# Performance work log

Measured on AMD Instinct MI355X. Metric: run time of the kernel, lower is better.

## Reference

```python
import jax, jax.numpy as jnp
import numpy as np

B, T, V = 4, 2048, 2048
D, H, L = 512, 8, 4
HD = D // H


def setup_inputs() -> dict:
    key = jax.random.key(0)
    ks = jax.random.split(key, 8)
    inp = {
        "x": jax.random.normal(ks[0], (B, T, V), dtype=jnp.float32),
        "token_embedding": jax.random.normal(ks[1], (D, V), dtype=jnp.float32),
        "position_embedding": jax.random.normal(ks[2], (T, D), dtype=jnp.float32),
        "Wk": jax.random.normal(ks[3], (L, D, D), dtype=jnp.float32),
        "Wq": jax.random.normal(ks[4], (L, D, D), dtype=jnp.float32),
        "Wv": jax.random.normal(ks[5], (L, D, D), dtype=jnp.float32),
        "Wp": jax.random.normal(ks[6], (L, D, D), dtype=jnp.float32),
        "readout": jax.random.normal(ks[7], (V, D), dtype=jnp.float32),
    }
    return inp


def _attention_block(h, wk, wq, wv, wp):
    # h: [B, T, D]; weights [D, D] (inner_dim == D since head_dim*num_heads == D)
    b, t, c = h.shape
    s = c ** (-0.5)

    def proj(w):
        # F.linear(h, w) = h @ w.T -> [B,T,D] -> [B,H,T,HD], scaled by C^{-1/2}
        return (jnp.einsum('btc,dc->btd', h, w) * s).reshape(b, t, H, HD).transpose(0, 2, 1, 3)

    q, k, v = proj(wq), proj(wk), proj(wv)
    scores = jnp.einsum('bhqd,bhkd->bhqk', q, k) * (HD ** (-0.5))  # [B,H,T,T]
    attn = jax.nn.softmax(scores, axis=-1)
    out = jnp.einsum('bhqk,bhkd->bhqd', attn, v)  # [B,H,T,HD]
    out = out.transpose(0, 2, 1, 3).reshape(b, t, c)
    # projection.size(-1) == inner_dim == D
    return jnp.einsum('btc,oc->bto', out, wp) * (c ** (-0.5))


def reference(x, token_embedding, position_embedding, Wk, Wq, Wv, Wp, readout):
    b, t, c = x.shape  # c == vocab_size
    tok = jnp.einsum('btv,dv->btd', x, token_embedding) * (c ** (-0.5))
    h = tok + position_embedding[:t]
    for l in range(L):
        h = _attention_block(h, Wk[l], Wq[l], Wv[l], Wp[l])
    # logits on last token; readout.size(-1) == D
    logits = jnp.einsum('bd,vd->bv', h[:, -1, :], readout) * (D ** (-0.5))
    return logits
```

## Files before the change

### kernel.cpp

```cpp
#include <hip/hip_runtime.h>
#include <math.h>

typedef __attribute__((ext_vector_type(4)))  float    f32x4;
typedef __attribute__((ext_vector_type(16))) float    f32x16;
typedef __attribute__((ext_vector_type(2)))  _Float16 f16x2;
typedef __attribute__((ext_vector_type(4)))  _Float16 f16x4;
typedef __attribute__((ext_vector_type(8)))  _Float16 f16x8;
typedef __attribute__((ext_vector_type(4)))  unsigned u32x4;

constexpr int Bc  = 4;
constexpr int Tc  = 2048;
constexpr int Vc  = 2048;
constexpr int Dc  = 512;
constexpr int Hc  = 8;
constexpr int HDc = 64;
constexpr int Lc  = 4;
constexpr size_t SZe = (size_t)Bc * Tc * Dc;

constexpr float SM_C = 12.0f;

__device__ __forceinline__ void gload_lds16(const _Float16* g, _Float16* s) {
    __builtin_amdgcn_global_load_lds(
        (const __attribute__((address_space(1))) void*)g,
        (__attribute__((address_space(3))) void*)s,
        16, 0, 0);
}

__device__ __forceinline__ unsigned cvt_pk_u(float a, float b) {
    return __builtin_bit_cast(unsigned, __builtin_amdgcn_cvt_pkrtz(a, b));
}

__global__ __launch_bounds__(256) void cvt_k(
    const float* __restrict__ in, _Float16* __restrict__ out, int n4)
{
    for (int i = blockIdx.x * 256 + threadIdx.x; i < n4; i += gridDim.x * 256) {
        float4 v = ((const float4*)in)[i];
        f16x4 h = {(_Float16)v.x, (_Float16)v.y, (_Float16)v.z, (_Float16)v.w};
        *(f16x4*)&out[(size_t)i * 4] = h;
    }
}

__global__ __launch_bounds__(256) void cvtW_k(
    const float* __restrict__ a, const float* __restrict__ b,
    const float* __restrict__ c, const float* __restrict__ d,
    _Float16* __restrict__ oa, _Float16* __restrict__ ob,
    _Float16* __restrict__ oc, _Float16* __restrict__ od, int n4)
{
    const float* in; _Float16* out;
    switch (blockIdx.y) {
        case 0:  in = a; out = oa; break;
        case 1:  in = b; out = ob; break;
        case 2:  in = c; out = oc; break;
        default: in = d; out = od; break;
    }
    for (int i = blockIdx.x * 256 + threadIdx.x; i < n4; i += gridDim.x * 256) {
        float4 v = ((const float4*)in)[i];
        f16x4 h = {(_Float16)v.x, (_Float16)v.y, (_Float16)v.z, (_Float16)v.w};
        *(f16x4*)&out[(size_t)i * 4] = h;
    }
}


template<bool QKV>
__global__ __launch_bounds__(256) void gemm_f16(
    const _Float16* __restrict__ A,
    const _Float16* __restrict__ W0, const _Float16* __restrict__ W1,
    const _Float16* __restrict__ W2,
    void* __restrict__ C0, const float* __restrict__ pos,
    int K, float scA, float scB, int mstep, int moff, int ybase)
{
    __shared__ __align__(16) _Float16 LA[2][128 * 64];
    __shared__ __align__(16) _Float16 LB[2][64 * 64];

    const int tid = threadIdx.x;
    const int w  = tid >> 6, l = tid & 63;
    const int li = l & 15,  lg = l >> 4;
    const int wm = w >> 1,  wn = w & 1;
    const int m0 = (blockIdx.x * mstep + moff) * 128;
    const int y  = blockIdx.y + ybase;

    int sec = 0, n0;
    const _Float16* Wb;
    if (QKV) {
        sec = y >> 3; n0 = (y & 7) * 64;
        Wb = (sec == 0) ? W0 : ((sec == 1) ? W1 : W2);
    } else {
        n0 = y * 64; Wb = W0;
    }
    const float scale = (sec == 0) ? scA : scB;

    const _Float16* srcA[4];
    const _Float16* srcB[2];
#pragma unroll
    for (int i = 0; i < 4; ++i) {
        const int d = i * 4096 + tid * 16;
        const int r = d >> 7, cb = (d & 127) ^ ((r & 7) << 4);
        srcA[i] = A + (size_t)(m0 + r) * K + (cb >> 1);
    }
#pragma unroll
    for (int i = 0; i < 2; ++i) {
        const int d = i * 4096 + tid * 16;
        const int r = d >> 7, cb = (d & 127) ^ ((r & 7) << 4);
        srcB[i] = Wb + (size_t)(n0 + r) * K + (cb >> 1);
    }

    auto stage = [&](int b) {
#pragma unroll
        for (int i = 0; i < 4; ++i) { gload_lds16(srcA[i], &LA[b][i * 2048 + tid * 8]); srcA[i] += 64; }
#pragma unroll
        for (int i = 0; i < 2; ++i) { gload_lds16(srcB[i], &LB[b][i * 2048 + tid * 8]); srcB[i] += 64; }
    };

    f32x4 acc[4][2];
#pragma unroll
    for (int i = 0; i < 4; ++i)
#pragma unroll
        for (int j = 0; j < 2; ++j) acc[i][j] = (f32x4){0.f, 0.f, 0.f, 0.f};

    auto compute = [&](int b) {
        const char* Ab = (const char*)&LA[b][0];
        const char* Bb = (const char*)&LB[b][0];
        f16x8 af[4][2], bf[2][2];
#pragma unroll
        for (int mb = 0; mb < 4; ++mb) {
            const int row = wm * 64 + mb * 16 + li, sz = (row & 7) << 4;
#pragma unroll
            for (int fi = 0; fi < 2; ++fi)
                af[mb][fi] = *(const f16x8*)(Ab + row * 128 + ((fi * 64 + lg * 16) ^ sz));
        }
#pragma unroll
        for (int nb = 0; nb < 2; ++nb) {
            const int row = wn * 32 + nb * 16 + li, sz = (row & 7) << 4;
#pragma unroll
            for (int fi = 0; fi < 2; ++fi)
                bf[nb][fi] = *(const f16x8*)(Bb + row * 128 + ((fi * 64 + lg * 16) ^ sz));
        }
#pragma unroll
        for (int mb = 0; mb < 4; ++mb)
#pragma unroll
            for (int nb = 0; nb < 2; ++nb)
#pragma unroll
                for (int fi = 0; fi < 2; ++fi)
                    acc[mb][nb] = __builtin_amdgcn_mfma_f32_16x16x32_f16(
                        af[mb][fi], bf[nb][fi], acc[mb][nb], 0, 0, 0);
    };

    const int NTk = K >> 6;
    stage(0);
    for (int kt = 0; kt < NTk; ++kt) {
        const int cur = kt & 1;
        if (kt + 1 < NTk) {
            stage(cur ^ 1);
            asm volatile("s_waitcnt vmcnt(6)" ::: "memory");
        } else {
            asm volatile("s_waitcnt vmcnt(0)" ::: "memory");
        }
        __builtin_amdgcn_s_barrier();
        __builtin_amdgcn_sched_barrier(0);
        compute(cur);
        __builtin_amdgcn_s_barrier();
        __builtin_amdgcn_sched_barrier(0);
    }

#pragma unroll
    for (int mb = 0; mb < 4; ++mb) {
#pragma unroll
        for (int nb = 0; nb < 2; ++nb) {
            const int mbase = m0 + wm * 64 + mb * 16 + lg * 4;
            const int nc    = n0 + wn * 32 + nb * 16 + li;
            if (QKV && sec == 2) {
                const int t0 = mbase & (Tc - 1);
                const int bh2 = (mbase >> 11) * Hc + (nc >> 6), d = nc & 63;
                f16x4 vv;
#pragma unroll
                for (int r = 0; r < 4; ++r) vv[r] = (_Float16)(acc[mb][nb][r] * scale);
                _Float16* vf = (_Float16*)C0 + 2 * SZe;
                const size_t adr =
                    (((size_t)bh2 * 32 + (t0 >> 6)) * 8 + (d >> 5) * 4 + ((t0 >> 4) & 3)) * 512
                    + ((d & 31) + 32 * ((t0 >> 3) & 1)) * 8 + (t0 & 7);
                *(f16x4*)&vf[adr] = vv;
            } else if (QKV && sec == 1) {
                _Float16* kf = (_Float16*)C0 + SZe;
                const int t0 = mbase & (Tc - 1);
                const int bh2 = (mbase >> 11) * Hc + (nc >> 6), d = nc & 63;
                const size_t adr0 =
                    (((size_t)bh2 * 32 + (t0 >> 6)) * 8 + ((t0 >> 5) & 1) * 4 + (d >> 4)) * 512
                    + ((t0 & 31) + 32 * ((d >> 3) & 1)) * 8 + (d & 7);
#pragma unroll
                for (int r = 0; r < 4; ++r)
                    kf[adr0 + (size_t)r * 8] = (_Float16)(acc[mb][nb][r] * scale);
            } else if (QKV) {
                _Float16* outp = (_Float16*)C0;
#pragma unroll
                for (int r = 0; r < 4; ++r) {
                    const int m = mbase + r, bb2 = m >> 11, t = m & (Tc - 1);
                    outp[(((size_t)bb2 * Hc + (nc >> 6)) * Tc + t) * HDc + (nc & 63)] =
                        (_Float16)(acc[mb][nb][r] * scale);
                }
            } else {
                _Float16* outp = (_Float16*)C0;
#pragma unroll
                for (int r = 0; r < 4; ++r) {
                    const int m = mbase + r;
                    float val = acc[mb][nb][r] * scale;
                    if (pos) val += pos[(size_t)(m & (Tc - 1)) * Dc + nc];
                    outp[(size_t)m * Dc + nc] = (_Float16)val;
                }
            }
        }
    }
}

__global__ __launch_bounds__(256) void attn_mfma(
    const _Float16* __restrict__ Qh, const _Float16* __restrict__ Kf,
    const _Float16* __restrict__ Vf, _Float16* __restrict__ o, int qtoff)
{
    __shared__ float cm[4224];

    const int bid = blockIdx.x;
    const int bh  = bid & 31;
    const int qt  = (bid >> 5) + qtoff;
    const int hh  = bh & (Hc - 1);
    const int bb  = bh >> 3;
    const int tid = threadIdx.x;
    const int w   = tid >> 6;
    const int l   = tid & 63;
    const int li  = l & 31, lg2 = l >> 5;
    const int qhalf = w & 1, khalf = w >> 1;
    const int q0  = qt * 64 + qhalf * 32;

    const _Float16* Qb = Qh + (size_t)bh * Tc * HDc;
    f16x8 qf[4];
#pragma unroll
    for (int fi = 0; fi < 4; ++fi)
        qf[fi] = *(const f16x8*)&Qb[(size_t)(q0 + li) * HDc + fi * 16 + lg2 * 8];

    const _Float16* Kb  = Kf + (size_t)bh * Tc * HDc + (khalf * 4) * 512 + l * 8;
    const _Float16* Vb0 = Vf + (size_t)bh * Tc * HDc + (khalf * 2) * 512 + l * 8;
    const _Float16* Vb1 = Vb0 + 4 * 512;

    f32x16 oacc0, oacc1, lacc, sinit;
#pragma unroll
    for (int i = 0; i < 16; ++i) { oacc0[i] = 0.f; oacc1[i] = 0.f; lacc[i] = 0.f; sinit[i] = -SM_C; }
    f16x8 ones;
#pragma unroll
    for (int i = 0; i < 8; ++i) ones[i] = (_Float16)1.f;

    f16x8 kfr[4], vfr[4];
#pragma unroll
    for (int fi = 0; fi < 4; ++fi) kfr[fi] = *(const f16x8*)(Kb + fi * 512);
#pragma unroll
    for (int m = 0; m < 2; ++m) {
        vfr[m]     = *(const f16x8*)(Vb0 + m * 512);
        vfr[2 + m] = *(const f16x8*)(Vb1 + m * 512);
    }
    Kb += 4096; Vb0 += 4096; Vb1 += 4096;

    constexpr int NT = Tc / 64;
    for (int kt = 0; kt < NT; ++kt) {
        __builtin_amdgcn_s_setprio(1);
        f32x16 s = __builtin_amdgcn_mfma_f32_32x32x16_f16(kfr[0], qf[0], sinit, 0, 0, 0);
        s = __builtin_amdgcn_mfma_f32_32x32x16_f16(kfr[1], qf[1], s, 0, 0, 0);
        s = __builtin_amdgcn_mfma_f32_32x32x16_f16(kfr[2], qf[2], s, 0, 0, 0);
        s = __builtin_amdgcn_mfma_f32_32x32x16_f16(kfr[3], qf[3], s, 0, 0, 0);
        __builtin_amdgcn_s_setprio(0);

        if (kt + 1 < NT) {
#pragma unroll
            for (int fi = 0; fi < 4; ++fi) kfr[fi] = *(const f16x8*)(Kb + fi * 512);
            Kb += 4096;
        }

        unsigned cc[8];
#pragma unroll
        for (int g = 0; g < 4; ++g) {
            float p0 = __builtin_amdgcn_exp2f(s[4 * g + 0]);
            float p1 = __builtin_amdgcn_exp2f(s[4 * g + 1]);
            float p2 = __builtin_amdgcn_exp2f(s[4 * g + 2]);
            float p3 = __builtin_amdgcn_exp2f(s[4 * g + 3]);
            cc[2 * g]     = cvt_pk_u(p0, p1);
            cc[2 * g + 1] = cvt_pk_u(p2, p3);
        }

        f16x8 Bf[2];
#pragma unroll
        for (int m = 0; m < 2; ++m) {
            auto u = __builtin_amdgcn_permlane32_swap(cc[m * 4 + 0], cc[m * 4 + 2], false, false);
            auto v = __builtin_amdgcn_permlane32_swap(cc[m * 4 + 1], cc[m * 4 + 3], false, false);
            u32x4 b4 = (u32x4){u[0], v[0], u[1], v[1]};
            Bf[m] = __builtin_bit_cast(f16x8, b4);
        }

        __builtin_amdgcn_s_setprio(1);
        lacc  = __builtin_amdgcn_mfma_f32_32x32x16_f16(ones,   Bf[0], lacc,  0, 0, 0);
        oacc0 = __builtin_amdgcn_mfma_f32_32x32x16_f16(vfr[0], Bf[0], oacc0, 0, 0, 0);
        oacc0 = __builtin_amdgcn_mfma_f32_32x32x16_f16(vfr[1], Bf[1], oacc0, 0, 0, 0);
        lacc  = __builtin_amdgcn_mfma_f32_32x32x16_f16(ones,   Bf[1], lacc,  0, 0, 0);
        oacc1 = __builtin_amdgcn_mfma_f32_32x32x16_f16(vfr[2], Bf[0], oacc1, 0, 0, 0);
        oacc1 = __builtin_amdgcn_mfma_f32_32x32x16_f16(vfr[3], Bf[1], oacc1, 0, 0, 0);
        __builtin_amdgcn_s_setprio(0);

        if (kt + 1 < NT) {
#pragma unroll
            for (int m = 0; m < 2; ++m) {
                vfr[m]     = *(const f16x8*)(Vb0 + m * 512);
                vfr[2 + m] = *(const f16x8*)(Vb1 + m * 512);
            }
            Vb0 += 4096; Vb1 += 4096;
        }
    }

    const float lrun_w = lacc[0];
    const int cbase = qhalf * (64 * 33) + l * 33;
    if (khalf == 1) {
#pragma unroll
        for (int i = 0; i < 16; ++i) cm[cbase + i]      = oacc0[i];
#pragma unroll
        for (int i = 0; i < 16; ++i) cm[cbase + 16 + i] = oacc1[i];
        cm[cbase + 32] = lrun_w;
    }
    __syncthreads();
    if (khalf == 0) {
#pragma unroll
        for (int i = 0; i < 16; ++i) oacc0[i] += cm[cbase + i];
#pragma unroll
        for (int i = 0; i < 16; ++i) oacc1[i] += cm[cbase + 16 + i];
        const float inv = 1.f / (lrun_w + cm[cbase + 32]);

        _Float16* op = o + ((size_t)(bb * Tc + q0 + li) * Dc + hh * HDc);
#pragma unroll
        for (int g = 0; g < 4; ++g) {
            const int d0 = 8 * g + 4 * lg2;
            f16x4 r0 = {(_Float16)(oacc0[4 * g + 0] * inv), (_Float16)(oacc0[4 * g + 1] * inv),
                        (_Float16)(oacc0[4 * g + 2] * inv), (_Float16)(oacc0[4 * g + 3] * inv)};
            f16x4 r1 = {(_Float16)(oacc1[4 * g + 0] * inv), (_Float16)(oacc1[4 * g + 1] * inv),
                        (_Float16)(oacc1[4 * g + 2] * inv), (_Float16)(oacc1[4 * g + 3] * inv)};
            *(f16x4*)(op + d0)      = r0;
            *(f16x4*)(op + 32 + d0) = r1;
        }
    }
}

__global__ __launch_bounds__(256) void readout_k(
    const _Float16* __restrict__ h, const float* __restrict__ ro,
    float* __restrict__ out, float scale)
{
    const int idx = blockIdx.x * 256 + threadIdx.x;
    const int vv  = idx & (Vc - 1);
    const int bb  = idx >> 11;
    const _Float16* hp = h + (size_t)(bb * Tc + (Tc - 1)) * Dc;
    const float* rp = ro + (size_t)vv * Dc;
    float ax = 0.f, ay = 0.f, az = 0.f, aw = 0.f;
#pragma unroll 8
    for (int i = 0; i < Dc / 4; ++i) {
        f16x4  hv = *(const f16x4*)(hp + i * 4);
        float4 rv = *(const float4*)(rp + i * 4);
        ax = fmaf((float)hv[0], rv.x, ax);
        ay = fmaf((float)hv[1], rv.y, ay);
        az = fmaf((float)hv[2], rv.z, az);
        aw = fmaf((float)hv[3], rv.w, aw);
    }
    out[idx] = ((ax + ay) + (az + aw)) * scale;
}

extern "C" void kernel_launch(void* const* d_in, const int* in_sizes, int n_in,
                              void* d_out, int out_size, void* d_ws, size_t ws_size,
                              hipStream_t stream)
{
    const float* x    = (const float*)d_in[0];
    const float* temb = (const float*)d_in[1];
    const float* pemb = (const float*)d_in[2];
    const float* Wk   = (const float*)d_in[3];
    const float* Wq   = (const float*)d_in[4];
    const float* Wv   = (const float*)d_in[5];
    const float* Wp   = (const float*)d_in[6];
    const float* ro   = (const float*)d_in[7];
    float* out = (float*)d_out;

    _Float16* h16    = (_Float16*)d_ws;
    _Float16* temb16 = h16 + SZe;
    _Float16* wq16   = temb16 + (size_t)Dc * Vc;
    _Float16* wk16   = wq16 + (size_t)Lc * Dc * Dc;
    _Float16* wv16   = wk16 + (size_t)Lc * Dc * Dc;
    _Float16* wp16   = wv16 + (size_t)Lc * Dc * Dc;
    _Float16* o16    = wp16 + (size_t)Lc * Dc * Dc;
    _Float16* qh     = o16 + SZe;
    _Float16* khF    = qh + SZe;
    _Float16* vhF    = khF + SZe;
    _Float16* x16    = o16;

    const float s_emb  = 1.0f / sqrtf((float)Vc);
    const float s_proj = 1.0f / sqrtf((float)Dc);
    const float s_q    = s_proj * 0.125f * 1.44269504f;

    const int W4 = Lc * Dc * Dc / 4;
    cvt_k<<<2048, 256, 0, stream>>>(x, x16, (int)SZe);
    cvt_k<<<512, 256, 0, stream>>>(temb, temb16, Dc * Vc / 4);
    cvtW_k<<<dim3(512, 4), 256, 0, stream>>>(Wq, Wk, Wv, Wp,
                                             wq16, wk16, wv16, wp16, W4);

    gemm_f16<false><<<dim3(64, 8), 256, 0, stream>>>(
        x16, temb16, nullptr, nullptr, h16, pemb, Vc, s_emb, s_emb, 1, 0, 0);

    const size_t WOFF = (size_t)Dc * Dc;
    for (int lyr = 0; lyr < Lc; ++lyr) {
        const bool last = (lyr == Lc - 1);
        if (!last) {
            gemm_f16<true><<<dim3(64, 24), 256, 0, stream>>>(
                h16, wq16 + lyr * WOFF, wk16 + lyr * WOFF, wv16 + lyr * WOFF,
                qh, nullptr, Dc, s_q, s_proj, 1, 0, 0);

            attn_mfma<<<Bc * Hc * (Tc / 64), 256, 0, stream>>>(qh, khF, vhF, o16, 0);

            gemm_f16<false><<<dim3(64, 8), 256, 0, stream>>>(
                o16, wp16 + lyr * WOFF, nullptr, nullptr, h16, nullptr,
                Dc, s_proj, s_proj, 1, 0, 0);
        } else {
            gemm_f16<true><<<dim3(64, 16), 256, 0, stream>>>(
                h16, wq16 + lyr * WOFF, wk16 + lyr * WOFF, wv16 + lyr * WOFF,
                qh, nullptr, Dc, s_q, s_proj, 1, 0, 8);
            gemm_f16<true><<<dim3(4, 8), 256, 0, stream>>>(
                h16, wq16 + lyr * WOFF, wk16 + lyr * WOFF, wv16 + lyr * WOFF,
                qh, nullptr, Dc, s_q, s_proj, 16, 15, 0);

            attn_mfma<<<Bc * Hc, 256, 0, stream>>>(qh, khF, vhF, o16, 31);

            gemm_f16<false><<<dim3(4, 8), 256, 0, stream>>>(
                o16, wp16 + lyr * WOFF, nullptr, nullptr, h16, nullptr,
                Dc, s_proj, s_proj, 16, 15, 0);
        }
    }

    readout_k<<<(Bc * Vc) / 256, 256, 0, stream>>>(h16, ro, out, s_proj);
}
```

Baseline: 383.0 us.

## Split attention key tiles across eight waves with two-stage LDS reduction

The attention kernel now runs 512 threads per block. The new set of four waves processes alternating 64-key tiles, so each wave walks half as many K/V tiles. Partial outputs and row sums are combined through two LDS reduction rounds before normalization and the store. This is meant to shorten the per-block serial loop and raise wave count for latency hiding. The cost is more register and LDS pressure per block, extra barriers, and possibly fewer resident blocks per CU.

```diff
diff --git a/kernel.cpp b/kernel.cpp
--- a/kernel.cpp
+++ b/kernel.cpp
@@ -211,11 +211,11 @@
     }
 }
 
-__global__ __launch_bounds__(256) void attn_mfma(
+__global__ __launch_bounds__(512) void attn_mfma(
     const _Float16* __restrict__ Qh, const _Float16* __restrict__ Kf,
     const _Float16* __restrict__ Vf, _Float16* __restrict__ o, int qtoff)
 {
-    __shared__ float cm[4224];
+    __shared__ float cm[4 * 64 * 33];
 
     const int bid = blockIdx.x;
     const int bh  = bid & 31;
@@ -226,7 +226,7 @@
     const int w   = tid >> 6;
     const int l   = tid & 63;
     const int li  = l & 31, lg2 = l >> 5;
-    const int qhalf = w & 1, khalf = w >> 1;
+    const int qhalf = w & 1, khalf = (w >> 1) & 1, ktp = w >> 2;
     const int q0  = qt * 64 + qhalf * 32;
 
     const _Float16* Qb = Qh + (size_t)bh * Tc * HDc;
@@ -235,8 +235,10 @@
     for (int fi = 0; fi < 4; ++fi)
         qf[fi] = *(const f16x8*)&Qb[(size_t)(q0 + li) * HDc + fi * 16 + lg2 * 8];
 
-    const _Float16* Kb  = Kf + (size_t)bh * Tc * HDc + (khalf * 4) * 512 + l * 8;
-    const _Float16* Vb0 = Vf + (size_t)bh * Tc * HDc + (khalf * 2) * 512 + l * 8;
+    const _Float16* Kb  = Kf + (size_t)bh * Tc * HDc + (size_t)ktp * 4096
+                          + (khalf * 4) * 512 + l * 8;
+    const _Float16* Vb0 = Vf + (size_t)bh * Tc * HDc + (size_t)ktp * 4096
+                          + (khalf * 2) * 512 + l * 8;
     const _Float16* Vb1 = Vb0 + 4 * 512;
 
     f32x16 oacc0, oacc1, lacc, sinit;
@@ -254,10 +256,10 @@
         vfr[m]     = *(const f16x8*)(Vb0 + m * 512);
         vfr[2 + m] = *(const f16x8*)(Vb1 + m * 512);
     }
-    Kb += 4096; Vb0 += 4096; Vb1 += 4096;
+    Kb += 8192; Vb0 += 8192; Vb1 += 8192;
 
     constexpr int NT = Tc / 64;
-    for (int kt = 0; kt < NT; ++kt) {
+    for (int kt = ktp; kt < NT; kt += 2) {
         __builtin_amdgcn_s_setprio(1);
         f32x16 s = __builtin_amdgcn_mfma_f32_32x32x16_f16(kfr[0], qf[0], sinit, 0, 0, 0);
         s = __builtin_amdgcn_mfma_f32_32x32x16_f16(kfr[1], qf[1], s, 0, 0, 0);
@@ -265,10 +267,10 @@
         s = __builtin_amdgcn_mfma_f32_32x32x16_f16(kfr[3], qf[3], s, 0, 0, 0);
         __builtin_amdgcn_s_setprio(0);
 
-        if (kt + 1 < NT) {
+        if (kt + 2 < NT) {
 #pragma unroll
             for (int fi = 0; fi < 4; ++fi) kfr[fi] = *(const f16x8*)(Kb + fi * 512);
-            Kb += 4096;
+            Kb += 8192;
         }
 
         unsigned cc[8];
@@ -300,32 +302,52 @@
         oacc1 = __builtin_amdgcn_mfma_f32_32x32x16_f16(vfr[3], Bf[1], oacc1, 0, 0, 0);
         __builtin_amdgcn_s_setprio(0);
 
-        if (kt + 1 < NT) {
+        if (kt + 2 < NT) {
 #pragma unroll
             for (int m = 0; m < 2; ++m) {
                 vfr[m]     = *(const f16x8*)(Vb0 + m * 512);
                 vfr[2 + m] = *(const f16x8*)(Vb1 + m * 512);
             }
-            Vb0 += 4096; Vb1 += 4096;
-        }
-    }
-
-    const float lrun_w = lacc[0];
-    const int cbase = qhalf * (64 * 33) + l * 33;
-    if (khalf == 1) {
-#pragma unroll
-        for (int i = 0; i < 16; ++i) cm[cbase + i]      = oacc0[i];
-#pragma unroll
-        for (int i = 0; i < 16; ++i) cm[cbase + 16 + i] = oacc1[i];
-        cm[cbase + 32] = lrun_w;
+            Vb0 += 8192; Vb1 += 8192;
+        }
+    }
+
+    float lrun = lacc[0];
+    const int slot = qhalf * 2 + khalf;
+    float* cs = cm + slot * (64 * 33) + l * 33;
+
+    if (ktp == 1) {
+#pragma unroll
+        for (int i = 0; i < 16; ++i) cs[i]      = oacc0[i];
+#pragma unroll
+        for (int i = 0; i < 16; ++i) cs[16 + i] = oacc1[i];
+        cs[32] = lrun;
     }
     __syncthreads();
-    if (khalf == 0) {
-#pragma unroll
-        for (int i = 0; i < 16; ++i) oacc0[i] += cm[cbase + i];
-#pragma unroll
-        for (int i = 0; i < 16; ++i) oacc1[i] += cm[cbase + 16 + i];
-        const float inv = 1.f / (lrun_w + cm[cbase + 32]);
+    if (ktp == 0) {
+#pragma unroll
+        for (int i = 0; i < 16; ++i) oacc0[i] += cs[i];
+#pragma unroll
+        for (int i = 0; i < 16; ++i) oacc1[i] += cs[16 + i];
+        lrun += cs[32];
+    }
+    __syncthreads();
+
+    float* cs2 = cm + (qhalf * 2 + 1) * (64 * 33) + l * 33;
+    if (ktp == 0 && khalf == 1) {
+#pragma unroll
+        for (int i = 0; i < 16; ++i) cs2[i]      = oacc0[i];
+#pragma unroll
+        for (int i = 0; i < 16; ++i) cs2[16 + i] = oacc1[i];
+        cs2[32] = lrun;
+    }
+    __syncthreads();
+    if (ktp == 0 && khalf == 0) {
+#pragma unroll
+        for (int i = 0; i < 16; ++i) oacc0[i] += cs2[i];
+#pragma unroll
+        for (int i = 0; i < 16; ++i) oacc1[i] += cs2[16 + i];
+        const float inv = 1.f / (lrun + cs2[32]);
 
         _Float16* op = o + ((size_t)(bb * Tc + q0 + li) * Dc + hh * HDc);
 #pragma unroll
@@ -410,7 +432,7 @@
                 h16, wq16 + lyr * WOFF, wk16 + lyr * WOFF, wv16 + lyr * WOFF,
                 qh, nullptr, Dc, s_q, s_proj, 1, 0, 0);
 
-            attn_mfma<<<Bc * Hc * (Tc / 64), 256, 0, stream>>>(qh, khF, vhF, o16, 0);
+            attn_mfma<<<Bc * Hc * (Tc / 64), 512, 0, stream>>>(qh, khF, vhF, o16, 0);
 
             gemm_f16<false><<<dim3(64, 8), 256, 0, stream>>>(
                 o16, wp16 + lyr * WOFF, nullptr, nullptr, h16, nullptr,
@@ -423,7 +445,7 @@
                 h16, wq16 + lyr * WOFF, wk16 + lyr * WOFF, wv16 + lyr * WOFF,
                 qh, nullptr, Dc, s_q, s_proj, 16, 15, 0);
 
-            attn_mfma<<<Bc * Hc, 256, 0, stream>>>(qh, khF, vhF, o16, 31);
+            attn_mfma<<<Bc * Hc, 512, 0, stream>>>(qh, khF, vhF, o16, 31);
 
             gemm_f16<false><<<dim3(4, 8), 256, 0, stream>>>(
                 o16, wp16 + lyr * WOFF, nullptr, nullptr, h16, nullptr,
```

Measured after the change: 381.0 us. No clear change (-0.5%).

## Halve GEMM M-tile to 64 rows and merge conversion kernels into one launch

Applied to the files above, without the earlier changes.

Shrinks the GEMM block tile from 128x64 to 64x64, so per-wave accumulators, LDS staging and the vmcnt wait count drop and the grid doubles. This gives more blocks to spread across the many CUs for these fairly small GEMMs (M=8192, N=512). The last-layer launches that compute only the final token's 64-row tile get updated mstep/moff values. The three fp32-to-fp16 conversion launches become a single 6-way kernel to cut launch overhead. The cost is lower per-block operand reuse and more global/L2 traffic for the weight tiles.

```diff
diff --git a/kernel.cpp b/kernel.cpp
--- a/kernel.cpp
+++ b/kernel.cpp
@@ -30,9 +30,23 @@
     return __builtin_bit_cast(unsigned, __builtin_amdgcn_cvt_pkrtz(a, b));
 }
 
-__global__ __launch_bounds__(256) void cvt_k(
-    const float* __restrict__ in, _Float16* __restrict__ out, int n4)
+__global__ __launch_bounds__(256) void cvtAll_k(
+    const float* __restrict__ x,  const float* __restrict__ temb,
+    const float* __restrict__ wq, const float* __restrict__ wk,
+    const float* __restrict__ wv, const float* __restrict__ wp,
+    _Float16* __restrict__ ox,  _Float16* __restrict__ otemb,
+    _Float16* __restrict__ owq, _Float16* __restrict__ owk,
+    _Float16* __restrict__ owv, _Float16* __restrict__ owp)
 {
+    const float* in; _Float16* out; int n4;
+    switch (blockIdx.y) {
+        case 0:  in = x;    out = ox;    n4 = (int)SZe;       break;
+        case 1:  in = temb; out = otemb; n4 = Dc * Vc / 4;    break;
+        case 2:  in = wq;   out = owq;   n4 = Lc * Dc * Dc / 4; break;
+        case 3:  in = wk;   out = owk;   n4 = Lc * Dc * Dc / 4; break;
+        case 4:  in = wv;   out = owv;   n4 = Lc * Dc * Dc / 4; break;
+        default: in = wp;   out = owp;   n4 = Lc * Dc * Dc / 4; break;
+    }
     for (int i = blockIdx.x * 256 + threadIdx.x; i < n4; i += gridDim.x * 256) {
         float4 v = ((const float4*)in)[i];
         f16x4 h = {(_Float16)v.x, (_Float16)v.y, (_Float16)v.z, (_Float16)v.w};
@@ -40,43 +54,23 @@
     }
 }
 
-__global__ __launch_bounds__(256) void cvtW_k(
-    const float* __restrict__ a, const float* __restrict__ b,
-    const float* __restrict__ c, const float* __restrict__ d,
-    _Float16* __restrict__ oa, _Float16* __restrict__ ob,
-    _Float16* __restrict__ oc, _Float16* __restrict__ od, int n4)
-{
-    const float* in; _Float16* out;
-    switch (blockIdx.y) {
-        case 0:  in = a; out = oa; break;
-        case 1:  in = b; out = ob; break;
-        case 2:  in = c; out = oc; break;
-        default: in = d; out = od; break;
-    }
-    for (int i = blockIdx.x * 256 + threadIdx.x; i < n4; i += gridDim.x * 256) {
-        float4 v = ((const float4*)in)[i];
-        f16x4 h = {(_Float16)v.x, (_Float16)v.y, (_Float16)v.z, (_Float16)v.w};
-        *(f16x4*)&out[(size_t)i * 4] = h;
-    }
-}
-
 
 template<bool QKV>
-__global__ __launch_bounds__(256) void gemm_f16(
+__global__ __launch_bounds__(256) void gemm64(
     const _Float16* __restrict__ A,
     const _Float16* __restrict__ W0, const _Float16* __restrict__ W1,
     const _Float16* __restrict__ W2,
     void* __restrict__ C0, const float* __restrict__ pos,
     int K, float scA, float scB, int mstep, int moff, int ybase)
 {
-    __shared__ __align__(16) _Float16 LA[2][128 * 64];
+    __shared__ __align__(16) _Float16 LA[2][64 * 64];
     __shared__ __align__(16) _Float16 LB[2][64 * 64];
 
     const int tid = threadIdx.x;
     const int w  = tid >> 6, l = tid & 63;
     const int li = l & 15,  lg = l >> 4;
     const int wm = w >> 1,  wn = w & 1;
-    const int m0 = (blockIdx.x * mstep + moff) * 128;
+    const int m0 = (blockIdx.x * mstep + moff) * 64;
     const int y  = blockIdx.y + ybase;
 
     int sec = 0, n0;
@@ -89,41 +83,36 @@
     }
     const float scale = (sec == 0) ? scA : scB;
 
-    const _Float16* srcA[4];
+    const _Float16* srcA[2];
     const _Float16* srcB[2];
-#pragma unroll
-    for (int i = 0; i < 4; ++i) {
-        const int d = i * 4096 + tid * 16;
-        const int r = d >> 7, cb = (d & 127) ^ ((r & 7) << 4);
-        srcA[i] = A + (size_t)(m0 + r) * K + (cb >> 1);
-    }
 #pragma unroll
     for (int i = 0; i < 2; ++i) {
         const int d = i * 4096 + tid * 16;
         const int r = d >> 7, cb = (d & 127) ^ ((r & 7) << 4);
+        srcA[i] = A  + (size_t)(m0 + r) * K + (cb >> 1);
         srcB[i] = Wb + (size_t)(n0 + r) * K + (cb >> 1);
     }
 
     auto stage = [&](int b) {
 #pragma unroll
-        for (int i = 0; i < 4; ++i) { gload_lds16(srcA[i], &LA[b][i * 2048 + tid * 8]); srcA[i] += 64; }
+        for (int i = 0; i < 2; ++i) { gload_lds16(srcA[i], &LA[b][i * 2048 + tid * 8]); srcA[i] += 64; }
 #pragma unroll
         for (int i = 0; i < 2; ++i) { gload_lds16(srcB[i], &LB[b][i * 2048 + tid * 8]); srcB[i] += 64; }
     };
 
-    f32x4 acc[4][2];
-#pragma unroll
-    for (int i = 0; i < 4; ++i)
+    f32x4 acc[2][2];
+#pragma unroll
+    for (int i = 0; i < 2; ++i)
 #pragma unroll
         for (int j = 0; j < 2; ++j) acc[i][j] = (f32x4){0.f, 0.f, 0.f, 0.f};
 
     auto compute = [&](int b) {
         const char* Ab = (const char*)&LA[b][0];
         const char* Bb = (const char*)&LB[b][0];
-        f16x8 af[4][2], bf[2][2];
-#pragma unroll
-        for (int mb = 0; mb < 4; ++mb) {
-            const int row = wm * 64 + mb * 16 + li, sz = (row & 7) << 4;
+        f16x8 af[2][2], bf[2][2];
+#pragma unroll
+        for (int mb = 0; mb < 2; ++mb) {
+            const int row = wm * 32 + mb * 16 + li, sz = (row & 7) << 4;
 #pragma unroll
             for (int fi = 0; fi < 2; ++fi)
                 af[mb][fi] = *(const f16x8*)(Ab + row * 128 + ((fi * 64 + lg * 16) ^ sz));
@@ -136,7 +125,7 @@
                 bf[nb][fi] = *(const f16x8*)(Bb + row * 128 + ((fi * 64 + lg * 16) ^ sz));
         }
 #pragma unroll
-        for (int mb = 0; mb < 4; ++mb)
+        for (int mb = 0; mb < 2; ++mb)
 #pragma unroll
             for (int nb = 0; nb < 2; ++nb)
 #pragma unroll
@@ -151,7 +140,7 @@
         const int cur = kt & 1;
         if (kt + 1 < NTk) {
             stage(cur ^ 1);
-            asm volatile("s_waitcnt vmcnt(6)" ::: "memory");
+            asm volatile("s_waitcnt vmcnt(4)" ::: "memory");
         } else {
             asm volatile("s_waitcnt vmcnt(0)" ::: "memory");
         }
@@ -163,10 +152,10 @@
     }
 
 #pragma unroll
-    for (int mb = 0; mb < 4; ++mb) {
+    for (int mb = 0; mb < 2; ++mb) {
 #pragma unroll
         for (int nb = 0; nb < 2; ++nb) {
-            const int mbase = m0 + wm * 64 + mb * 16 + lg * 4;
+            const int mbase = m0 + wm * 32 + mb * 16 + lg * 4;
             const int nc    = n0 + wn * 32 + nb * 16 + li;
             if (QKV && sec == 2) {
                 const int t0 = mbase & (Tc - 1);
@@ -393,41 +382,38 @@
     const float s_proj = 1.0f / sqrtf((float)Dc);
     const float s_q    = s_proj * 0.125f * 1.44269504f;
 
-    const int W4 = Lc * Dc * Dc / 4;
-    cvt_k<<<2048, 256, 0, stream>>>(x, x16, (int)SZe);
-    cvt_k<<<512, 256, 0, stream>>>(temb, temb16, Dc * Vc / 4);
-    cvtW_k<<<dim3(512, 4), 256, 0, stream>>>(Wq, Wk, Wv, Wp,
-                                             wq16, wk16, wv16, wp16, W4);
-
-    gemm_f16<false><<<dim3(64, 8), 256, 0, stream>>>(
+    cvtAll_k<<<dim3(1024, 6), 256, 0, stream>>>(
+        x, temb, Wq, Wk, Wv, Wp, x16, temb16, wq16, wk16, wv16, wp16);
+
+    gemm64<false><<<dim3(128, 8), 256, 0, stream>>>(
         x16, temb16, nullptr, nullptr, h16, pemb, Vc, s_emb, s_emb, 1, 0, 0);
 
     const size_t WOFF = (size_t)Dc * Dc;
     for (int lyr = 0; lyr < Lc; ++lyr) {
         const bool last = (lyr == Lc - 1);
         if (!last) {
-            gemm_f16<true><<<dim3(64, 24), 256, 0, stream>>>(
+            gemm64<true><<<dim3(128, 24), 256, 0, stream>>>(
                 h16, wq16 + lyr * WOFF, wk16 + lyr * WOFF, wv16 + lyr * WOFF,
                 qh, nullptr, Dc, s_q, s_proj, 1, 0, 0);
 
             attn_mfma<<<Bc * Hc * (Tc / 64), 256, 0, stream>>>(qh, khF, vhF, o16, 0);
 
-            gemm_f16<false><<<dim3(64, 8), 256, 0, stream>>>(
+            gemm64<false><<<dim3(128, 8), 256, 0, stream>>>(
                 o16, wp16 + lyr * WOFF, nullptr, nullptr, h16, nullptr,
                 Dc, s_proj, s_proj, 1, 0, 0);
         } else {
-            gemm_f16<true><<<dim3(64, 16), 256, 0, stream>>>(
+            gemm64<true><<<dim3(128, 16), 256, 0, stream>>>(
                 h16, wq16 + lyr * WOFF, wk16 + lyr * WOFF, wv16 + lyr * WOFF,
                 qh, nullptr, Dc, s_q, s_proj, 1, 0, 8);
-            gemm_f16<true><<<dim3(4, 8), 256, 0, stream>>>(
+            gemm64<true><<<dim3(4, 8), 256, 0, stream>>>(
                 h16, wq16 + lyr * WOFF, wk16 + lyr * WOFF, wv16 + lyr * WOFF,
-                qh, nullptr, Dc, s_q, s_proj, 16, 15, 0);
+                qh, nullptr, Dc, s_q, s_proj, 32, 31, 0);
 
             attn_mfma<<<Bc * Hc, 256, 0, stream>>>(qh, khF, vhF, o16, 31);
 
-            gemm_f16<false><<<dim3(4, 8), 256, 0, stream>>>(
+            gemm64<false><<<dim3(4, 8), 256, 0, stream>>>(
                 o16, wp16 + lyr * WOFF, nullptr, nullptr, h16, nullptr,
-                Dc, s_proj, s_proj, 16, 15, 0);
+                Dc, s_proj, s_proj, 32, 31, 0);
         }
     }
 
```

New measurement: 372.6 us. -2.7%, faster.
